# Optimization experiments

Measured on AMD Instinct MI355X. Metric: run time of the kernel, lower is better.

## Reference

```python
import jax, jax.numpy as jnp
import numpy as np

DIM = 768
NUM_HEADS = 12
HEAD_DIM = DIM // NUM_HEADS
EPS = 1e-6  # flax nn.LayerNorm default


def layer_norm(x, scale, bias):
    # LayerNorm over last axis (head_dim)
    mean = jnp.mean(x, axis=-1, keepdims=True)
    var = jnp.var(x, axis=-1, keepdims=True)
    return (x - mean) * jax.lax.rsqrt(var + EPS) * scale + bias


def setup_inputs() -> dict:
    key = jax.random.key(0)
    k0, = jax.random.split(key, 1)
    B, N = 4, 2048
    QKV = jax.random.normal(k0, (B, N, 3 * DIM), dtype=jnp.float32)
    return {
        "QKV": QKV,
        "q_scale": jnp.ones((HEAD_DIM,), jnp.float32),
        "q_bias": jnp.zeros((HEAD_DIM,), jnp.float32),
        "k_scale": jnp.ones((HEAD_DIM,), jnp.float32),
        "k_bias": jnp.zeros((HEAD_DIM,), jnp.float32),
    }


def reference(QKV, q_scale, q_bias, k_scale, k_bias):
    B, N, C = QKV.shape
    qkv = QKV.reshape(B, N, 3, NUM_HEADS, HEAD_DIM)
    qkv = jnp.transpose(qkv, (2, 0, 3, 1, 4))  # [3, B, H, N, d]
    q, k, v = qkv[0], qkv[1], qkv[2]
    q = layer_norm(q, q_scale, q_bias)
    k = layer_norm(k, k_scale, k_bias)
    attn = jnp.einsum('bhqd,bhkd->bhqk', q, k) * (HEAD_DIM ** -0.5)
    attn = jax.nn.softmax(attn, axis=-1)
    x = jnp.einsum('bhqk,bhkd->bhqd', attn, v)
    return x
```

## Files before the change

kernel.cpp:

```cpp
#include <hip/hip_runtime.h>
#include <math.h>

#define NB   4
#define SEQ  2048
#define NH   12
#define CIN  2304
#define TM   64
#define NCH  (SEQ/TM)
#define TQ   128

typedef _Float16 half8 __attribute__((ext_vector_type(8)));
typedef _Float16 half4 __attribute__((ext_vector_type(4)));
typedef float    f32x4 __attribute__((ext_vector_type(4)));

__global__ __launch_bounds__(256, 3)
void fused_ln_attn(const float* __restrict__ QKV,
                   const float* __restrict__ q_scale,
                   const float* __restrict__ q_bias,
                   const float* __restrict__ k_scale,
                   const float* __restrict__ k_bias,
                   float* __restrict__ out)
{
    __shared__ __align__(16) unsigned char sm[32768];
    unsigned char* Ka = sm;
    unsigned char* Vt = sm + 8192;
    unsigned char* Qt = sm + 16384;

    const int tid  = threadIdx.x;
    const int L    = tid & 63;
    const int wv   = tid >> 6;
    const int n16  = L & 15;
    const int quad = L >> 4;
    const int sw   = n16 & 7;
    const int r4   = L >> 2;
    const int c4   = L & 3;

    const int id  = blockIdx.x;
    const int xcd = id & 7;
    const int qt  = (id >> 3) & 15;
    const int grp = id >> 7;
    const int bh  = grp * 8 + xcd;
    const int b   = bh / NH;
    const int h   = bh - b * NH;
    const int q0  = qt * TQ;

    const float4* QKV4 = (const float4*)QKV;
    unsigned char* Pw = Qt + wv * 4096;

    float4 ksr[4], kbr[4];
    #pragma unroll
    for (int i = 0; i < 4; ++i) {
        ksr[i] = ((const float4*)k_scale)[c4 * 4 + i];
        kbr[i] = ((const float4*)k_bias)[c4 * 4 + i];
    }

    float4 kx[4];
    float  vv[16];
    {
        const size_t kb4 = (size_t)(b*SEQ + wv*16 + r4) * 576 + 192 + h*16 + c4*4;
        #pragma unroll
        for (int i = 0; i < 4; ++i) kx[i] = QKV4[kb4 + i];
        const float* gv = QKV + (size_t)(b*SEQ + wv*16) * CIN + 1536 + h*64 + L;
        #pragma unroll
        for (int j = 0; j < 16; ++j) vv[j] = gv[(size_t)j * CIN];
    }

    #pragma unroll
    for (int g = 0; g < 2; ++g) {
        const int row = wv*32 + g*16 + r4;
        const size_t base4 = (size_t)(b*SEQ + q0 + row) * 576 + h*16 + c4*4;
        float4 x[4];
        #pragma unroll
        for (int i = 0; i < 4; ++i) x[i] = QKV4[base4 + i];
        float s = 0.f, s2 = 0.f;
        #pragma unroll
        for (int i = 0; i < 4; ++i) {
            s  += x[i].x + x[i].y + x[i].z + x[i].w;
            s2 += x[i].x*x[i].x + x[i].y*x[i].y + x[i].z*x[i].z + x[i].w*x[i].w;
        }
        s  += __shfl_xor(s, 1);  s  += __shfl_xor(s, 2);
        s2 += __shfl_xor(s2, 1); s2 += __shfl_xor(s2, 2);
        float mu = s * 0.015625f;
        float rstd = rsqrtf(s2 * 0.015625f - mu*mu + 1e-6f);
        float nb0 = -mu * rstd;
        half8 h0, h1;
        #pragma unroll
        for (int i = 0; i < 4; ++i) {
            float4 sc = ((const float4*)q_scale)[c4*4 + i];
            float4 bi = ((const float4*)q_bias)[c4*4 + i];
            float e0 = (fmaf(x[i].x, rstd, nb0) * sc.x + bi.x) * 0.125f;
            float e1 = (fmaf(x[i].y, rstd, nb0) * sc.y + bi.y) * 0.125f;
            float e2 = (fmaf(x[i].z, rstd, nb0) * sc.z + bi.z) * 0.125f;
            float e3 = (fmaf(x[i].w, rstd, nb0) * sc.w + bi.w) * 0.125f;
            if (i < 2) { h0[i*4+0]=(_Float16)e0; h0[i*4+1]=(_Float16)e1; h0[i*4+2]=(_Float16)e2; h0[i*4+3]=(_Float16)e3; }
            else { int j=(i-2)*4; h1[j+0]=(_Float16)e0; h1[j+1]=(_Float16)e1; h1[j+2]=(_Float16)e2; h1[j+3]=(_Float16)e3; }
        }
        *(half8*)(Qt + row*128 + (((2*c4+0) ^ (r4 & 7)) * 16)) = h0;
        *(half8*)(Qt + row*128 + (((2*c4+1) ^ (r4 & 7)) * 16)) = h1;
    }

    half8 qf[2][2];
    #pragma unroll
    for (int s = 0; s < 2; ++s) {
        const unsigned char* qrow = Qt + (wv*32 + s*16 + n16)*128;
        #pragma unroll
        for (int ks = 0; ks < 2; ++ks)
            qf[s][ks] = *(const half8*)(qrow + (((quad + 4*ks) ^ sw) * 16));
    }

    f32x4 oacc[2][4] = {};
    float lsum[2] = {0.f, 0.f};

    for (int mc = 0; mc < NCH; ++mc) {
        __syncthreads();

        {
            const int row = wv*16 + r4;
            float s = 0.f, s2 = 0.f;
            #pragma unroll
            for (int i = 0; i < 4; ++i) {
                s  += kx[i].x + kx[i].y + kx[i].z + kx[i].w;
                s2 += kx[i].x*kx[i].x + kx[i].y*kx[i].y + kx[i].z*kx[i].z + kx[i].w*kx[i].w;
            }
            s  += __shfl_xor(s, 1);  s  += __shfl_xor(s, 2);
            s2 += __shfl_xor(s2, 1); s2 += __shfl_xor(s2, 2);
            float mu = s * 0.015625f;
            float rstd = rsqrtf(s2 * 0.015625f - mu*mu + 1e-6f);
            float nb0 = -mu * rstd;
            half8 h0, h1;
            #pragma unroll
            for (int i = 0; i < 4; ++i) {
                float e0 = fmaf(kx[i].x, rstd, nb0) * ksr[i].x + kbr[i].x;
                float e1 = fmaf(kx[i].y, rstd, nb0) * ksr[i].y + kbr[i].y;
                float e2 = fmaf(kx[i].z, rstd, nb0) * ksr[i].z + kbr[i].z;
                float e3 = fmaf(kx[i].w, rstd, nb0) * ksr[i].w + kbr[i].w;
                if (i < 2) { h0[i*4+0]=(_Float16)e0; h0[i*4+1]=(_Float16)e1; h0[i*4+2]=(_Float16)e2; h0[i*4+3]=(_Float16)e3; }
                else { int j=(i-2)*4; h1[j+0]=(_Float16)e0; h1[j+1]=(_Float16)e1; h1[j+2]=(_Float16)e2; h1[j+3]=(_Float16)e3; }
            }
            *(half8*)(Ka + row*128 + (((2*c4+0) ^ (row & 7)) * 16)) = h0;
            *(half8*)(Ka + row*128 + (((2*c4+1) ^ (row & 7)) * 16)) = h1;
        }
        {
            half8 a0, a1;
            #pragma unroll
            for (int j = 0; j < 8; ++j) { a0[j] = (_Float16)vv[j]; a1[j] = (_Float16)vv[j+8]; }
            *(half8*)(Vt + L*128 + (((2*wv+0) ^ (L & 7)) * 16)) = a0;
            *(half8*)(Vt + L*128 + (((2*wv+1) ^ (L & 7)) * 16)) = a1;
        }
        __syncthreads();

        if (mc + 1 < NCH) {
            const size_t kb4 = (size_t)(b*SEQ + (mc+1)*64 + wv*16 + r4) * 576 + 192 + h*16 + c4*4;
            #pragma unroll
            for (int i = 0; i < 4; ++i) kx[i] = QKV4[kb4 + i];
            const float* gv = QKV + (size_t)(b*SEQ + (mc+1)*64 + wv*16) * CIN + 1536 + h*64 + L;
            #pragma unroll
            for (int j = 0; j < 16; ++j) vv[j] = gv[(size_t)j * CIN];
        }

        f32x4 sacc[2][4] = {};
        #pragma unroll
        for (int ks = 0; ks < 2; ++ks) {
            half8 ak[4];
            #pragma unroll
            for (int mt = 0; mt < 4; ++mt)
                ak[mt] = *(const half8*)(Ka + (16*mt + n16)*128 + (((quad + 4*ks) ^ sw) * 16));
            #pragma unroll
            for (int s = 0; s < 2; ++s)
                #pragma unroll
                for (int mt = 0; mt < 4; ++mt)
                    sacc[s][mt] = __builtin_amdgcn_mfma_f32_16x16x32_f16(ak[mt], qf[s][ks], sacc[s][mt], 0, 0, 0);
        }

        #pragma unroll
        for (int s = 0; s < 2; ++s) {
            float ls = 0.f;
            #pragma unroll
            for (int mt = 0; mt < 4; ++mt) {
                float p0 = __expf(sacc[s][mt][0]);
                float p1 = __expf(sacc[s][mt][1]);
                float p2 = __expf(sacc[s][mt][2]);
                float p3 = __expf(sacc[s][mt][3]);
                ls += (p0 + p1) + (p2 + p3);
                half4 hp; hp[0]=(_Float16)p0; hp[1]=(_Float16)p1; hp[2]=(_Float16)p2; hp[3]=(_Float16)p3;
                *(half4*)(Pw + s*2048 + n16*128 + (((4*mt + quad) ^ n16) * 8)) = hp;
            }
            ls += __shfl_xor(ls, 16);
            ls += __shfl_xor(ls, 32);
            lsum[s] += ls;
        }

        #pragma unroll
        for (int ks = 0; ks < 2; ++ks) {
            half8 av[4];
            #pragma unroll
            for (int mt = 0; mt < 4; ++mt)
                av[mt] = *(const half8*)(Vt + (16*mt + n16)*128 + (((quad + 4*ks) ^ sw) * 16));
            #pragma unroll
            for (int s = 0; s < 2; ++s) {
                half4 b0 = *(const half4*)(Pw + s*2048 + n16*128 + (((8*ks + 2*quad + 0) ^ n16) * 8));
                half4 b1 = *(const half4*)(Pw + s*2048 + n16*128 + (((8*ks + 2*quad + 1) ^ n16) * 8));
                half8 bp;
                #pragma unroll
                for (int j = 0; j < 4; ++j) { bp[j] = b0[j]; bp[4+j] = b1[j]; }
                #pragma unroll
                for (int mt = 0; mt < 4; ++mt)
                    oacc[s][mt] = __builtin_amdgcn_mfma_f32_16x16x32_f16(av[mt], bp, oacc[s][mt], 0, 0, 0);
            }
        }
    }

    float4* out4 = (float4*)out;
    #pragma unroll
    for (int s = 0; s < 2; ++s) {
        float inv = 1.0f / lsum[s];
        size_t rowb = ((size_t)(b*NH + h)*SEQ + q0 + wv*32 + s*16 + n16) * 16;
        #pragma unroll
        for (int mt = 0; mt < 4; ++mt)
            out4[rowb + mt*4 + quad] = make_float4(oacc[s][mt][0]*inv, oacc[s][mt][1]*inv,
                                                   oacc[s][mt][2]*inv, oacc[s][mt][3]*inv);
    }
}

extern "C" void kernel_launch(void* const* d_in, const int* in_sizes, int n_in,
                              void* d_out, int out_size, void* d_ws, size_t ws_size,
                              hipStream_t stream) {
    const float* QKV     = (const float*)d_in[0];
    const float* q_scale = (const float*)d_in[1];
    const float* q_bias  = (const float*)d_in[2];
    const float* k_scale = (const float*)d_in[3];
    const float* k_bias  = (const float*)d_in[4];
    float* out = (float*)d_out;

    fused_ln_attn<<<dim3(NB * NH * (SEQ / TQ)), 256, 0, stream>>>(
        QKV, q_scale, q_bias, k_scale, k_bias, out);
}
```

Baseline: 259.5 us.

## Halve query tile to 64 rows per block and use exp2 with folded log2e

Shrinks the query tile per block from 128 to 64 rows, so each wave handles one 16-row slab instead of two. This halves registers and shared memory per block, doubles the grid, and raises the occupancy hint from 3 to 6 blocks per CU. Each K/V chunk is now loaded and layer-normed once per 64 query rows instead of 128, doubling that global traffic and LN work. Separately, log2(e) is folded into the Q scale so the softmax can call exp2 directly.

```diff
diff --git a/kernel.cpp b/kernel.cpp
--- a/kernel.cpp
+++ b/kernel.cpp
@@ -7,13 +7,13 @@
 #define CIN  2304
 #define TM   64
 #define NCH  (SEQ/TM)
-#define TQ   128
+#define TQ   64
 
 typedef _Float16 half8 __attribute__((ext_vector_type(8)));
 typedef _Float16 half4 __attribute__((ext_vector_type(4)));
 typedef float    f32x4 __attribute__((ext_vector_type(4)));
 
-__global__ __launch_bounds__(256, 3)
+__global__ __launch_bounds__(256, 6)
 void fused_ln_attn(const float* __restrict__ QKV,
                    const float* __restrict__ q_scale,
                    const float* __restrict__ q_bias,
@@ -21,7 +21,7 @@
                    const float* __restrict__ k_bias,
                    float* __restrict__ out)
 {
-    __shared__ __align__(16) unsigned char sm[32768];
+    __shared__ __align__(16) unsigned char sm[24576];
     unsigned char* Ka = sm;
     unsigned char* Vt = sm + 8192;
     unsigned char* Qt = sm + 16384;
@@ -37,15 +37,15 @@
 
     const int id  = blockIdx.x;
     const int xcd = id & 7;
-    const int qt  = (id >> 3) & 15;
-    const int grp = id >> 7;
+    const int qt  = (id >> 3) & 31;
+    const int grp = id >> 8;
     const int bh  = grp * 8 + xcd;
     const int b   = bh / NH;
     const int h   = bh - b * NH;
     const int q0  = qt * TQ;
 
     const float4* QKV4 = (const float4*)QKV;
-    unsigned char* Pw = Qt + wv * 4096;
+    unsigned char* Pw = Qt + wv * 2048;
 
     float4 ksr[4], kbr[4];
     #pragma unroll
@@ -65,9 +65,8 @@
         for (int j = 0; j < 16; ++j) vv[j] = gv[(size_t)j * CIN];
     }
 
-    #pragma unroll
-    for (int g = 0; g < 2; ++g) {
-        const int row = wv*32 + g*16 + r4;
+    {
+        const int row = wv*16 + r4;
         const size_t base4 = (size_t)(b*SEQ + q0 + row) * 576 + h*16 + c4*4;
         float4 x[4];
         #pragma unroll
@@ -83,15 +82,16 @@
         float mu = s * 0.015625f;
         float rstd = rsqrtf(s2 * 0.015625f - mu*mu + 1e-6f);
         float nb0 = -mu * rstd;
+        const float SC = 0.125f * 1.44269504088896340736f;
         half8 h0, h1;
         #pragma unroll
         for (int i = 0; i < 4; ++i) {
             float4 sc = ((const float4*)q_scale)[c4*4 + i];
             float4 bi = ((const float4*)q_bias)[c4*4 + i];
-            float e0 = (fmaf(x[i].x, rstd, nb0) * sc.x + bi.x) * 0.125f;
-            float e1 = (fmaf(x[i].y, rstd, nb0) * sc.y + bi.y) * 0.125f;
-            float e2 = (fmaf(x[i].z, rstd, nb0) * sc.z + bi.z) * 0.125f;
-            float e3 = (fmaf(x[i].w, rstd, nb0) * sc.w + bi.w) * 0.125f;
+            float e0 = (fmaf(x[i].x, rstd, nb0) * sc.x + bi.x) * SC;
+            float e1 = (fmaf(x[i].y, rstd, nb0) * sc.y + bi.y) * SC;
+            float e2 = (fmaf(x[i].z, rstd, nb0) * sc.z + bi.z) * SC;
+            float e3 = (fmaf(x[i].w, rstd, nb0) * sc.w + bi.w) * SC;
             if (i < 2) { h0[i*4+0]=(_Float16)e0; h0[i*4+1]=(_Float16)e1; h0[i*4+2]=(_Float16)e2; h0[i*4+3]=(_Float16)e3; }
             else { int j=(i-2)*4; h1[j+0]=(_Float16)e0; h1[j+1]=(_Float16)e1; h1[j+2]=(_Float16)e2; h1[j+3]=(_Float16)e3; }
         }
@@ -99,17 +99,16 @@
         *(half8*)(Qt + row*128 + (((2*c4+1) ^ (r4 & 7)) * 16)) = h1;
     }
 
-    half8 qf[2][2];
-    #pragma unroll
-    for (int s = 0; s < 2; ++s) {
-        const unsigned char* qrow = Qt + (wv*32 + s*16 + n16)*128;
+    half8 qf[2];
+    {
+        const unsigned char* qrow = Qt + (wv*16 + n16)*128;
         #pragma unroll
         for (int ks = 0; ks < 2; ++ks)
-            qf[s][ks] = *(const half8*)(qrow + (((quad + 4*ks) ^ sw) * 16));
-    }
-
-    f32x4 oacc[2][4] = {};
-    float lsum[2] = {0.f, 0.f};
+            qf[ks] = *(const half8*)(qrow + (((quad + 4*ks) ^ sw) * 16));
+    }
+
+    f32x4 oacc[4] = {};
+    float lsum = 0.f;
 
     for (int mc = 0; mc < NCH; ++mc) {
         __syncthreads();
@@ -158,68 +157,55 @@
             for (int j = 0; j < 16; ++j) vv[j] = gv[(size_t)j * CIN];
         }
 
-        f32x4 sacc[2][4] = {};
+        f32x4 sacc[4] = {};
         #pragma unroll
         for (int ks = 0; ks < 2; ++ks) {
-            half8 ak[4];
-            #pragma unroll
-            for (int mt = 0; mt < 4; ++mt)
-                ak[mt] = *(const half8*)(Ka + (16*mt + n16)*128 + (((quad + 4*ks) ^ sw) * 16));
-            #pragma unroll
-            for (int s = 0; s < 2; ++s)
-                #pragma unroll
-                for (int mt = 0; mt < 4; ++mt)
-                    sacc[s][mt] = __builtin_amdgcn_mfma_f32_16x16x32_f16(ak[mt], qf[s][ks], sacc[s][mt], 0, 0, 0);
-        }
-
-        #pragma unroll
-        for (int s = 0; s < 2; ++s) {
+            #pragma unroll
+            for (int mt = 0; mt < 4; ++mt) {
+                half8 ak = *(const half8*)(Ka + (16*mt + n16)*128 + (((quad + 4*ks) ^ sw) * 16));
+                sacc[mt] = __builtin_amdgcn_mfma_f32_16x16x32_f16(ak, qf[ks], sacc[mt], 0, 0, 0);
+            }
+        }
+
+        {
             float ls = 0.f;
             #pragma unroll
             for (int mt = 0; mt < 4; ++mt) {
-                float p0 = __expf(sacc[s][mt][0]);
-                float p1 = __expf(sacc[s][mt][1]);
-                float p2 = __expf(sacc[s][mt][2]);
-                float p3 = __expf(sacc[s][mt][3]);
+                float p0 = __builtin_exp2f(sacc[mt][0]);
+                float p1 = __builtin_exp2f(sacc[mt][1]);
+                float p2 = __builtin_exp2f(sacc[mt][2]);
+                float p3 = __builtin_exp2f(sacc[mt][3]);
                 ls += (p0 + p1) + (p2 + p3);
                 half4 hp; hp[0]=(_Float16)p0; hp[1]=(_Float16)p1; hp[2]=(_Float16)p2; hp[3]=(_Float16)p3;
-                *(half4*)(Pw + s*2048 + n16*128 + (((4*mt + quad) ^ n16) * 8)) = hp;
+                *(half4*)(Pw + n16*128 + (((4*mt + quad) ^ n16) * 8)) = hp;
             }
             ls += __shfl_xor(ls, 16);
             ls += __shfl_xor(ls, 32);
-            lsum[s] += ls;
+            lsum += ls;
         }
 
         #pragma unroll
         for (int ks = 0; ks < 2; ++ks) {
-            half8 av[4];
-            #pragma unroll
-            for (int mt = 0; mt < 4; ++mt)
-                av[mt] = *(const half8*)(Vt + (16*mt + n16)*128 + (((quad + 4*ks) ^ sw) * 16));
-            #pragma unroll
-            for (int s = 0; s < 2; ++s) {
-                half4 b0 = *(const half4*)(Pw + s*2048 + n16*128 + (((8*ks + 2*quad + 0) ^ n16) * 8));
-                half4 b1 = *(const half4*)(Pw + s*2048 + n16*128 + (((8*ks + 2*quad + 1) ^ n16) * 8));
-                half8 bp;
-                #pragma unroll
-                for (int j = 0; j < 4; ++j) { bp[j] = b0[j]; bp[4+j] = b1[j]; }
-                #pragma unroll
-                for (int mt = 0; mt < 4; ++mt)
-                    oacc[s][mt] = __builtin_amdgcn_mfma_f32_16x16x32_f16(av[mt], bp, oacc[s][mt], 0, 0, 0);
-            }
-        }
-    }
-
+            half4 b0 = *(const half4*)(Pw + n16*128 + (((8*ks + 2*quad + 0) ^ n16) * 8));
+            half4 b1 = *(const half4*)(Pw + n16*128 + (((8*ks + 2*quad + 1) ^ n16) * 8));
+            half8 bp;
+            #pragma unroll
+            for (int j = 0; j < 4; ++j) { bp[j] = b0[j]; bp[4+j] = b1[j]; }
+            #pragma unroll
+            for (int mt = 0; mt < 4; ++mt) {
+                half8 av = *(const half8*)(Vt + (16*mt + n16)*128 + (((quad + 4*ks) ^ sw) * 16));
+                oacc[mt] = __builtin_amdgcn_mfma_f32_16x16x32_f16(av, bp, oacc[mt], 0, 0, 0);
+            }
+        }
+    }
+
+    float inv = 1.0f / lsum;
     float4* out4 = (float4*)out;
+    size_t rowb = ((size_t)(b*NH + h)*SEQ + q0 + wv*16 + n16) * 16;
     #pragma unroll
-    for (int s = 0; s < 2; ++s) {
-        float inv = 1.0f / lsum[s];
-        size_t rowb = ((size_t)(b*NH + h)*SEQ + q0 + wv*32 + s*16 + n16) * 16;
-        #pragma unroll
-        for (int mt = 0; mt < 4; ++mt)
-            out4[rowb + mt*4 + quad] = make_float4(oacc[s][mt][0]*inv, oacc[s][mt][1]*inv,
-                                                   oacc[s][mt][2]*inv, oacc[s][mt][3]*inv);
-    }
+    for (int mt = 0; mt < 4; ++mt)
+        out4[rowb + mt*4 + quad] = make_float4(oacc[mt][0]*inv, oacc[mt][1]*inv,
+                                               oacc[mt][2]*inv, oacc[mt][3]*inv);
 }
 
 extern "C" void kernel_launch(void* const* d_in, const int* in_sizes, int n_in,
```

New measurement: 594.8 us. 129% more time.

## Double-buffer K/V tiles in LDS and fold log2e into Q scale

Applied to the files above, without the earlier changes.

Splits the K/V shared-memory staging into two buffers so the next chunk is layer-normed and written while the current chunk is consumed, with global prefetch two chunks ahead. This cuts the loop from two barriers per iteration to one. It also folds log2(e) into the Q scaling and uses exp2 in place of exp, avoiding a multiply per score. LDS grows from 32 KB to 48 KB per block, which may lower occupancy below the 3 blocks per CU that the launch bounds request.

```diff
diff --git a/kernel.cpp b/kernel.cpp
--- a/kernel.cpp
+++ b/kernel.cpp
@@ -21,10 +21,8 @@
                    const float* __restrict__ k_bias,
                    float* __restrict__ out)
 {
-    __shared__ __align__(16) unsigned char sm[32768];
-    unsigned char* Ka = sm;
-    unsigned char* Vt = sm + 8192;
-    unsigned char* Qt = sm + 16384;
+    __shared__ __align__(16) unsigned char sm[49152];
+    unsigned char* Qt = sm + 32768;
 
     const int tid  = threadIdx.x;
     const int L    = tid & 63;
@@ -56,15 +54,54 @@
 
     float4 kx[4];
     float  vv[16];
-    {
-        const size_t kb4 = (size_t)(b*SEQ + wv*16 + r4) * 576 + 192 + h*16 + c4*4;
-        #pragma unroll
-        for (int i = 0; i < 4; ++i) kx[i] = QKV4[kb4 + i];
-        const float* gv = QKV + (size_t)(b*SEQ + wv*16) * CIN + 1536 + h*64 + L;
-        #pragma unroll
-        for (int j = 0; j < 16; ++j) vv[j] = gv[(size_t)j * CIN];
-    }
-
+    #define PREFETCH(MC)                                                          \
+    {                                                                             \
+        const size_t kb4 = (size_t)(b*SEQ + (MC)*64 + wv*16 + r4) * 576 + 192 + h*16 + c4*4; \
+        _Pragma("unroll")                                                         \
+        for (int i = 0; i < 4; ++i) kx[i] = QKV4[kb4 + i];                        \
+        const float* gv = QKV + (size_t)(b*SEQ + (MC)*64 + wv*16) * CIN + 1536 + h*64 + L; \
+        _Pragma("unroll")                                                         \
+        for (int j = 0; j < 16; ++j) vv[j] = gv[(size_t)j * CIN];                 \
+    }
+
+    #define STAGE(P)                                                              \
+    {                                                                             \
+        unsigned char* Ka_ = sm + (P)*16384;                                      \
+        unsigned char* Vt_ = Ka_ + 8192;                                          \
+        const int row = wv*16 + r4;                                               \
+        float s = 0.f, s2 = 0.f;                                                  \
+        _Pragma("unroll")                                                         \
+        for (int i = 0; i < 4; ++i) {                                             \
+            s  += kx[i].x + kx[i].y + kx[i].z + kx[i].w;                          \
+            s2 += kx[i].x*kx[i].x + kx[i].y*kx[i].y + kx[i].z*kx[i].z + kx[i].w*kx[i].w; \
+        }                                                                         \
+        s  += __shfl_xor(s, 1);  s  += __shfl_xor(s, 2);                          \
+        s2 += __shfl_xor(s2, 1); s2 += __shfl_xor(s2, 2);                         \
+        float mu = s * 0.015625f;                                                 \
+        float rstd = rsqrtf(s2 * 0.015625f - mu*mu + 1e-6f);                      \
+        float nb0 = -mu * rstd;                                                   \
+        half8 h0, h1;                                                             \
+        _Pragma("unroll")                                                         \
+        for (int i = 0; i < 4; ++i) {                                             \
+            float e0 = fmaf(kx[i].x, rstd, nb0) * ksr[i].x + kbr[i].x;            \
+            float e1 = fmaf(kx[i].y, rstd, nb0) * ksr[i].y + kbr[i].y;            \
+            float e2 = fmaf(kx[i].z, rstd, nb0) * ksr[i].z + kbr[i].z;            \
+            float e3 = fmaf(kx[i].w, rstd, nb0) * ksr[i].w + kbr[i].w;            \
+            if (i < 2) { h0[i*4+0]=(_Float16)e0; h0[i*4+1]=(_Float16)e1; h0[i*4+2]=(_Float16)e2; h0[i*4+3]=(_Float16)e3; } \
+            else { int j=(i-2)*4; h1[j+0]=(_Float16)e0; h1[j+1]=(_Float16)e1; h1[j+2]=(_Float16)e2; h1[j+3]=(_Float16)e3; } \
+        }                                                                         \
+        *(half8*)(Ka_ + row*128 + (((2*c4+0) ^ (row & 7)) * 16)) = h0;            \
+        *(half8*)(Ka_ + row*128 + (((2*c4+1) ^ (row & 7)) * 16)) = h1;            \
+        half8 a0, a1;                                                             \
+        _Pragma("unroll")                                                         \
+        for (int j = 0; j < 8; ++j) { a0[j] = (_Float16)vv[j]; a1[j] = (_Float16)vv[j+8]; } \
+        *(half8*)(Vt_ + L*128 + (((2*wv+0) ^ (L & 7)) * 16)) = a0;                \
+        *(half8*)(Vt_ + L*128 + (((2*wv+1) ^ (L & 7)) * 16)) = a1;                \
+    }
+
+    PREFETCH(0)
+
+    const float SC = 0.125f * 1.44269504088896340736f;
     #pragma unroll
     for (int g = 0; g < 2; ++g) {
         const int row = wv*32 + g*16 + r4;
@@ -88,10 +125,10 @@
         for (int i = 0; i < 4; ++i) {
             float4 sc = ((const float4*)q_scale)[c4*4 + i];
             float4 bi = ((const float4*)q_bias)[c4*4 + i];
-            float e0 = (fmaf(x[i].x, rstd, nb0) * sc.x + bi.x) * 0.125f;
-            float e1 = (fmaf(x[i].y, rstd, nb0) * sc.y + bi.y) * 0.125f;
-            float e2 = (fmaf(x[i].z, rstd, nb0) * sc.z + bi.z) * 0.125f;
-            float e3 = (fmaf(x[i].w, rstd, nb0) * sc.w + bi.w) * 0.125f;
+            float e0 = (fmaf(x[i].x, rstd, nb0) * sc.x + bi.x) * SC;
+            float e1 = (fmaf(x[i].y, rstd, nb0) * sc.y + bi.y) * SC;
+            float e2 = (fmaf(x[i].z, rstd, nb0) * sc.z + bi.z) * SC;
+            float e3 = (fmaf(x[i].w, rstd, nb0) * sc.w + bi.w) * SC;
             if (i < 2) { h0[i*4+0]=(_Float16)e0; h0[i*4+1]=(_Float16)e1; h0[i*4+2]=(_Float16)e2; h0[i*4+3]=(_Float16)e3; }
             else { int j=(i-2)*4; h1[j+0]=(_Float16)e0; h1[j+1]=(_Float16)e1; h1[j+2]=(_Float16)e2; h1[j+3]=(_Float16)e3; }
         }
@@ -108,55 +145,21 @@
             qf[s][ks] = *(const half8*)(qrow + (((quad + 4*ks) ^ sw) * 16));
     }
 
+    STAGE(0)
+    PREFETCH(1)
+    __syncthreads();
+
     f32x4 oacc[2][4] = {};
     float lsum[2] = {0.f, 0.f};
 
     for (int mc = 0; mc < NCH; ++mc) {
-        __syncthreads();
-
-        {
-            const int row = wv*16 + r4;
-            float s = 0.f, s2 = 0.f;
-            #pragma unroll
-            for (int i = 0; i < 4; ++i) {
-                s  += kx[i].x + kx[i].y + kx[i].z + kx[i].w;
-                s2 += kx[i].x*kx[i].x + kx[i].y*kx[i].y + kx[i].z*kx[i].z + kx[i].w*kx[i].w;
-            }
-            s  += __shfl_xor(s, 1);  s  += __shfl_xor(s, 2);
-            s2 += __shfl_xor(s2, 1); s2 += __shfl_xor(s2, 2);
-            float mu = s * 0.015625f;
-            float rstd = rsqrtf(s2 * 0.015625f - mu*mu + 1e-6f);
-            float nb0 = -mu * rstd;
-            half8 h0, h1;
-            #pragma unroll
-            for (int i = 0; i < 4; ++i) {
-                float e0 = fmaf(kx[i].x, rstd, nb0) * ksr[i].x + kbr[i].x;
-                float e1 = fmaf(kx[i].y, rstd, nb0) * ksr[i].y + kbr[i].y;
-                float e2 = fmaf(kx[i].z, rstd, nb0) * ksr[i].z + kbr[i].z;
-                float e3 = fmaf(kx[i].w, rstd, nb0) * ksr[i].w + kbr[i].w;
-                if (i < 2) { h0[i*4+0]=(_Float16)e0; h0[i*4+1]=(_Float16)e1; h0[i*4+2]=(_Float16)e2; h0[i*4+3]=(_Float16)e3; }
-                else { int j=(i-2)*4; h1[j+0]=(_Float16)e0; h1[j+1]=(_Float16)e1; h1[j+2]=(_Float16)e2; h1[j+3]=(_Float16)e3; }
-            }
-            *(half8*)(Ka + row*128 + (((2*c4+0) ^ (row & 7)) * 16)) = h0;
-            *(half8*)(Ka + row*128 + (((2*c4+1) ^ (row & 7)) * 16)) = h1;
-        }
-        {
-            half8 a0, a1;
-            #pragma unroll
-            for (int j = 0; j < 8; ++j) { a0[j] = (_Float16)vv[j]; a1[j] = (_Float16)vv[j+8]; }
-            *(half8*)(Vt + L*128 + (((2*wv+0) ^ (L & 7)) * 16)) = a0;
-            *(half8*)(Vt + L*128 + (((2*wv+1) ^ (L & 7)) * 16)) = a1;
-        }
-        __syncthreads();
-
-        if (mc + 1 < NCH) {
-            const size_t kb4 = (size_t)(b*SEQ + (mc+1)*64 + wv*16 + r4) * 576 + 192 + h*16 + c4*4;
-            #pragma unroll
-            for (int i = 0; i < 4; ++i) kx[i] = QKV4[kb4 + i];
-            const float* gv = QKV + (size_t)(b*SEQ + (mc+1)*64 + wv*16) * CIN + 1536 + h*64 + L;
-            #pragma unroll
-            for (int j = 0; j < 16; ++j) vv[j] = gv[(size_t)j * CIN];
-        }
+        const int p = mc & 1;
+
+        if (mc + 1 < NCH) STAGE(p ^ 1)
+        if (mc + 2 < NCH) PREFETCH(mc + 2)
+
+        const unsigned char* Ka = sm + p*16384;
+        const unsigned char* Vt = Ka + 8192;
 
         f32x4 sacc[2][4] = {};
         #pragma unroll
@@ -177,10 +180,10 @@
             float ls = 0.f;
             #pragma unroll
             for (int mt = 0; mt < 4; ++mt) {
-                float p0 = __expf(sacc[s][mt][0]);
-                float p1 = __expf(sacc[s][mt][1]);
-                float p2 = __expf(sacc[s][mt][2]);
-                float p3 = __expf(sacc[s][mt][3]);
+                float p0 = __builtin_exp2f(sacc[s][mt][0]);
+                float p1 = __builtin_exp2f(sacc[s][mt][1]);
+                float p2 = __builtin_exp2f(sacc[s][mt][2]);
+                float p3 = __builtin_exp2f(sacc[s][mt][3]);
                 ls += (p0 + p1) + (p2 + p3);
                 half4 hp; hp[0]=(_Float16)p0; hp[1]=(_Float16)p1; hp[2]=(_Float16)p2; hp[3]=(_Float16)p3;
                 *(half4*)(Pw + s*2048 + n16*128 + (((4*mt + quad) ^ n16) * 8)) = hp;
@@ -208,6 +211,8 @@
                     oacc[s][mt] = __builtin_amdgcn_mfma_f32_16x16x32_f16(av[mt], bp, oacc[s][mt], 0, 0, 0);
             }
         }
+
+        __syncthreads();
     }
 
     float4* out4 = (float4*)out;
```

Result: slower. 279.9 us (+7.9%).
